# Kernel tuning notes

Hardware: AMD Instinct MI355X
Metric: run time of the kernel (lower is better)

Reference implementation:

```python
import jax, jax.numpy as jnp
import numpy as np

N_NODES = 100000
N_EDGES = 1600000
D_IN = 128
D_HID = 128
D_OUT = 32


def setup_inputs() -> dict:
    key = jax.random.key(0)
    ks = jax.random.split(key, 10)
    x = jax.random.normal(ks[0], (N_NODES, D_IN), dtype=jnp.float32)
    edge_index = jax.random.randint(ks[1], (2, N_EDGES), 0, N_NODES, dtype=jnp.int64)
    s = 0.05
    return {
        "x": x,
        "edge_index": edge_index,
        "Wl0": jax.random.normal(ks[2], (D_IN, D_HID), jnp.float32) * s,
        "bl0": jnp.zeros((D_HID,), jnp.float32),
        "Wr0": jax.random.normal(ks[3], (D_IN, D_HID), jnp.float32) * s,
        "Wl1": jax.random.normal(ks[4], (D_HID, D_HID), jnp.float32) * s,
        "bl1": jnp.zeros((D_HID,), jnp.float32),
        "Wr1": jax.random.normal(ks[5], (D_HID, D_HID), jnp.float32) * s,
        "Wl2": jax.random.normal(ks[6], (D_HID, D_OUT), jnp.float32) * s,
        "bl2": jnp.zeros((D_OUT,), jnp.float32),
        "Wr2": jax.random.normal(ks[7], (D_HID, D_OUT), jnp.float32) * s,
    }


def _sage_conv(x, src, dst, Wl, bl, Wr):
    # PyG SAGEConv (aggr='mean', root_weight=True):
    # out[i] = lin_l(mean_{j in N(i)} x_j) + lin_r(x_i)
    n = x.shape[0]
    msgs = x[src]                                        # [E, F] gather
    agg = jax.ops.segment_sum(msgs, dst, num_segments=n) # [N, F] scatter-add
    deg = jax.ops.segment_sum(jnp.ones((src.shape[0],), x.dtype), dst, num_segments=n)
    mean = agg / jnp.maximum(deg, 1.0)[:, None]
    return mean @ Wl + bl + x @ Wr


def reference(x, edge_index, Wl0, bl0, Wr0, Wl1, bl1, Wr1, Wl2, bl2, Wr2):
    src, dst = edge_index[0], edge_index[1]
    h = jax.nn.relu(_sage_conv(x, src, dst, Wl0, bl0, Wr0))
    h = jax.nn.relu(_sage_conv(h, src, dst, Wl1, bl1, Wr1))
    h = _sage_conv(h, src, dst, Wl2, bl2, Wr2)
    return jax.nn.log_softmax(h, axis=1)
```

## Files before the change

kernel.cpp:

```cpp
#include <hip/hip_runtime.h>
#include <hip/hip_bf16.h>
#include <math.h>

#define NN 100000
#define NE 1600000

#define NCB 391
#define EB  4096
#define SCT 512
#define HBK 64
#define NSB 391
#define WPB 144

typedef __attribute__((ext_vector_type(8))) short short8;
typedef __attribute__((ext_vector_type(4))) float f32x4;

__device__ __forceinline__ unsigned short f2bf(float f) {
  union { float f; unsigned int i; } v; v.f = f;
  unsigned int i = v.i;
  unsigned int r = (i + 0x7FFFu + ((i >> 16) & 1u)) >> 16;
  return (unsigned short)r;
}
__device__ __forceinline__ float bflo(unsigned int u) {
  union { unsigned int i; float f; } v; v.i = u << 16; return v.f;
}
__device__ __forceinline__ float bfhi(unsigned int u) {
  union { unsigned int i; float f; } v; v.i = u & 0xFFFF0000u; return v.f;
}
__device__ __forceinline__ float bf1(unsigned short u) {
  union { unsigned int i; float f; } v; v.i = ((unsigned int)u) << 16; return v.f;
}

__global__ __launch_bounds__(512) void k_prep(
    const int* __restrict__ dst, int* __restrict__ bcnt,
    const float* __restrict__ Wl0, const float* __restrict__ Wr0,
    const float* __restrict__ Wl1, const float* __restrict__ Wr1,
    const float* __restrict__ Wl2, const float* __restrict__ Wr2,
    unsigned short* __restrict__ B0, unsigned short* __restrict__ B1,
    unsigned short* __restrict__ B2) {
  if (blockIdx.x < HBK) {
    __shared__ int h[NCB];
    for (int i = threadIdx.x; i < NCB; i += 512) h[i] = 0;
    __syncthreads();
    int stride = HBK * 512;
    for (int e = blockIdx.x * 512 + threadIdx.x; e < NE; e += stride) {
      int d = dst[e];
      d = d < 0 ? 0 : (d >= NN ? NN - 1 : d);
      atomicAdd(&h[d >> 8], 1);
    }
    __syncthreads();
    for (int i = threadIdx.x; i < NCB; i += 512) {
      int v = h[i];
      if (v) atomicAdd(&bcnt[i], v);
    }
  } else {
    int idx = (blockIdx.x - HBK) * 512 + threadIdx.x;
    if (idx < 32768) {
      int n = idx >> 7, k = idx & 127;
      float v = (n < 128) ? Wl0[k * 128 + n] : Wr0[k * 128 + (n - 128)];
      B0[idx] = f2bf(v);
    } else if (idx < 65536) {
      int j = idx - 32768;
      int n = j >> 7, k = j & 127;
      float v = (n < 128) ? Wl1[k * 128 + n] : Wr1[k * 128 + (n - 128)];
      B1[j] = f2bf(v);
    } else if (idx < 73728) {
      int j = idx - 65536;
      int n = j >> 7, k = j & 127;
      float v = (n < 32) ? Wl2[k * 32 + n] : Wr2[k * 32 + (n - 32)];
      B2[j] = f2bf(v);
    }
  }
}

__global__ __launch_bounds__(512) void k_cscan(const int* __restrict__ bcnt,
                                               int* __restrict__ cboff,
                                               int* __restrict__ csroff) {
  __shared__ int sd[512];
  int t = threadIdx.x;
  int v = (t < NCB) ? bcnt[t] : 0;
  sd[t] = v;
  __syncthreads();
  for (int st = 1; st < 512; st <<= 1) {
    int x = (t >= st) ? sd[t - st] : 0;
    __syncthreads();
    sd[t] += x;
    __syncthreads();
  }
  if (t < NCB) cboff[t] = sd[t] - v;
  if (t == NCB - 1) { cboff[NCB] = sd[t]; csroff[NN] = sd[t]; }
}

__device__ __forceinline__ void cscatter_body(
    char* smem, int bid,
    const int* __restrict__ src, const int* __restrict__ dst,
    const int* __restrict__ cboff, int* __restrict__ ccur,
    unsigned int* __restrict__ ebuf) {
  int* lh = (int*)smem;
  unsigned int* sRank = (unsigned int*)(smem + 1600);
  unsigned int* sPay  = (unsigned int*)(smem + 1600 + EB * 4);
  int t = threadIdx.x;
  int base = bid * EB;
  for (int i = t; i < NCB; i += SCT) lh[i] = 0;
  __syncthreads();
  #pragma unroll
  for (int i = 0; i < EB / SCT; i++) {
    int idx = i * SCT + t;
    int e = base + idx;
    unsigned int rk = 0xFFFFFFFFu, pv = 0;
    if (e < NE) {
      int d = dst[e];
      d = d < 0 ? 0 : (d >= NN ? NN - 1 : d);
      int s = src[e];
      s = s < 0 ? 0 : (s >= NN ? NN - 1 : s);
      int cb = d >> 8;
      int r = atomicAdd(&lh[cb], 1);
      rk = (((unsigned int)cb) << 13) | (unsigned int)r;
      pv = (((unsigned int)(d & 255)) << 17) | (unsigned int)s;
    }
    sRank[idx] = rk;
    sPay[idx]  = pv;
  }
  __syncthreads();
  for (int i = t; i < NCB; i += SCT) {
    int c = lh[i];
    int g = c ? atomicAdd(&ccur[i], c) : 0;
    lh[i] = cboff[i] + g;
  }
  __syncthreads();
  #pragma unroll
  for (int i = 0; i < EB / SCT; i++) {
    int idx = i * SCT + t;
    unsigned int rk = sRank[idx];
    if (rk != 0xFFFFFFFFu) {
      int cb = rk >> 13;
      int r  = rk & 0x1FFF;
      ebuf[lh[cb] + r] = sPay[idx];
    }
  }
}

__device__ __forceinline__ void mgemm0_body(
    char* smem, int bid, const float* __restrict__ A,
    const unsigned short* __restrict__ Bp, const float* __restrict__ bias,
    unsigned short* __restrict__ yl, unsigned short* __restrict__ yr) {
  unsigned short* sA = (unsigned short*)smem;
  int tid = threadIdx.x;
  int nb  = bid * 128;

  #pragma unroll
  for (int i = 0; i < 8; i++) {
    int j = i * 512 + tid;
    int m = j >> 5;
    int k4 = (j & 31) * 4;
    int gn = nb + m;
    float4 v = make_float4(0.f, 0.f, 0.f, 0.f);
    if (gn < NN) v = *(const float4*)&A[gn * 128 + k4];
    unsigned int p0 = (unsigned int)f2bf(v.x) | ((unsigned int)f2bf(v.y) << 16);
    unsigned int p1 = (unsigned int)f2bf(v.z) | ((unsigned int)f2bf(v.w) << 16);
    *(uint2*)&sA[m * 136 + k4] = make_uint2(p0, p1);
  }
  __syncthreads();

  int wave = tid >> 6, lane = tid & 63;
  int l15 = lane & 15, lq = lane >> 4;
  int wm = wave & 1, wn = wave >> 1;
  int mbase = wm * 64;
  int nbase = wn * 64;

  f32x4 acc[4][4];
  #pragma unroll
  for (int mi = 0; mi < 4; mi++)
    #pragma unroll
    for (int ni = 0; ni < 4; ni++) acc[mi][ni] = (f32x4){0.f, 0.f, 0.f, 0.f};

  #pragma unroll
  for (int kc = 0; kc < 4; kc++) {
    int k0 = kc * 32 + lq * 8;
    short8 af[4], bfr[4];
    #pragma unroll
    for (int ni = 0; ni < 4; ni++)
      bfr[ni] = *(const short8*)&Bp[(nbase + ni * 16 + l15) * 128 + k0];
    #pragma unroll
    for (int mi = 0; mi < 4; mi++)
      af[mi] = *(const short8*)&sA[(mbase + mi * 16 + l15) * 136 + k0];
    #pragma unroll
    for (int mi = 0; mi < 4; mi++)
      #pragma unroll
      for (int ni = 0; ni < 4; ni++)
        acc[mi][ni] = __builtin_amdgcn_mfma_f32_16x16x32_bf16(
            af[mi], bfr[ni], acc[mi][ni], 0, 0, 0);
  }

  #pragma unroll
  for (int mi = 0; mi < 4; mi++) {
    #pragma unroll
    for (int ni = 0; ni < 4; ni++) {
      int n = nbase + ni * 16 + l15;
      #pragma unroll
      for (int r = 0; r < 4; r++) {
        int gn = nb + mbase + mi * 16 + lq * 4 + r;
        if (gn < NN) {
          float v = acc[mi][ni][r];
          if (n < 128) {
            yl[(size_t)gn * 128 + n] = f2bf(v);
          } else {
            int n2 = n - 128;
            yr[(size_t)gn * 128 + n2] = f2bf(v + bias[n2]);
          }
        }
      }
    }
  }
}

__global__ __launch_bounds__(512) void k_scatgemm(
    const int* __restrict__ src, const int* __restrict__ dst,
    const int* __restrict__ cboff, int* __restrict__ ccur,
    unsigned int* __restrict__ ebuf,
    const float* __restrict__ x, const unsigned short* __restrict__ B0,
    const float* __restrict__ bias,
    unsigned short* __restrict__ yl, unsigned short* __restrict__ yr) {
  __shared__ char smem[128 * 136 * 2];
  if (blockIdx.x < NSB) {
    cscatter_body(smem, blockIdx.x, src, dst, cboff, ccur, ebuf);
  } else {
    mgemm0_body(smem, blockIdx.x - NSB, x, B0, bias, yl, yr);
  }
}

__global__ __launch_bounds__(512) void k_crefine(
    const unsigned int* __restrict__ ebuf, const int* __restrict__ cboff,
    int* __restrict__ csroff, float* __restrict__ invd,
    int* __restrict__ csrsrc) {
  __shared__ int lh[256], pos[256], cur[256];
  int b = blockIdx.x, t = threadIdx.x;
  if (t < 256) { lh[t] = 0; cur[t] = 0; }
  __syncthreads();
  int beg = cboff[b], end = cboff[b + 1];
  for (int i = beg + t; i < end; i += 512) atomicAdd(&lh[ebuf[i] >> 17], 1);
  __syncthreads();
  int v = (t < 256) ? lh[t] : 0;
  if (t < 256) pos[t] = v;
  __syncthreads();
  for (int st = 1; st < 256; st <<= 1) {
    int x = (t >= st && t < 256) ? pos[t - st] : 0;
    __syncthreads();
    if (t < 256) pos[t] += x;
    __syncthreads();
  }
  if (t < 256) {
    int nid = b * 256 + t;
    int mybase = cboff[b] + pos[t] - v;
    if (nid < NN) {
      csroff[nid] = mybase;
      invd[nid] = 1.0f / (float)(v < 1 ? 1 : v);
    }
    pos[t] = mybase;
  }
  __syncthreads();
  for (int i = beg + t; i < end; i += 512) {
    unsigned int u = ebuf[i];
    int local = u >> 17;
    int r = atomicAdd(&cur[local], 1);
    csrsrc[pos[local] + r] = (int)(u & 0x1FFFFu);
  }
}

template <int NC>
__global__ __launch_bounds__(512) void k_mgemm(
    const unsigned short* __restrict__ A, const unsigned short* __restrict__ Bp,
    const float* __restrict__ bias,
    unsigned short* __restrict__ yl, unsigned short* __restrict__ yr) {
  __shared__ unsigned short sA[128 * 136];
  int tid = threadIdx.x;
  int nb  = blockIdx.x * 128;

  #pragma unroll
  for (int i = 0; i < 4; i++) {
    int j = i * 512 + tid;
    int m = j >> 4;
    int k8 = (j & 15) * 8;
    int gn = nb + m;
    uint4 v = make_uint4(0, 0, 0, 0);
    if (gn < NN) v = *(const uint4*)&A[gn * 128 + k8];
    *(uint4*)&sA[m * 136 + k8] = v;
  }
  __syncthreads();

  int wave = tid >> 6, lane = tid & 63;
  int l15 = lane & 15, lq = lane >> 4;
  constexpr int MT = (NC == 256) ? 4 : 2;
  constexpr int NT = (NC == 256) ? 4 : 2;
  int wm, wn;
  if (NC == 256) { wm = wave & 1; wn = wave >> 1; }
  else           { wm = wave >> 1; wn = wave & 1; }
  int mbase = wm * (MT * 16);
  int nbase = wn * (NT * 16);

  f32x4 acc[MT][NT];
  #pragma unroll
  for (int mi = 0; mi < MT; mi++)
    #pragma unroll
    for (int ni = 0; ni < NT; ni++) acc[mi][ni] = (f32x4){0.f, 0.f, 0.f, 0.f};

  #pragma unroll
  for (int kc = 0; kc < 4; kc++) {
    int k0 = kc * 32 + lq * 8;
    short8 af[MT], bfr[NT];
    #pragma unroll
    for (int ni = 0; ni < NT; ni++)
      bfr[ni] = *(const short8*)&Bp[(nbase + ni * 16 + l15) * 128 + k0];
    #pragma unroll
    for (int mi = 0; mi < MT; mi++)
      af[mi] = *(const short8*)&sA[(mbase + mi * 16 + l15) * 136 + k0];
    #pragma unroll
    for (int mi = 0; mi < MT; mi++)
      #pragma unroll
      for (int ni = 0; ni < NT; ni++)
        acc[mi][ni] = __builtin_amdgcn_mfma_f32_16x16x32_bf16(
            af[mi], bfr[ni], acc[mi][ni], 0, 0, 0);
  }

  constexpr int HC = NC / 2;
  #pragma unroll
  for (int mi = 0; mi < MT; mi++) {
    #pragma unroll
    for (int ni = 0; ni < NT; ni++) {
      int n = nbase + ni * 16 + l15;
      #pragma unroll
      for (int r = 0; r < 4; r++) {
        int gn = nb + mbase + mi * 16 + lq * 4 + r;
        if (gn < NN) {
          float v = acc[mi][ni][r];
          if (n < HC) {
            yl[(size_t)gn * HC + n] = f2bf(v);
          } else {
            int n2 = n - HC;
            yr[(size_t)gn * HC + n2] = f2bf(v + bias[n2]);
          }
        }
      }
    }
  }
}

__global__ __launch_bounds__(256) void k_agg128(
    const unsigned short* __restrict__ yl, const unsigned short* __restrict__ yr,
    const int* __restrict__ off, const int* __restrict__ csr,
    const float* __restrict__ invd, unsigned short* __restrict__ out, int relu) {
  int wid  = (blockIdx.x * 256 + threadIdx.x) >> 6;
  int lane = threadIdx.x & 63;
  if (wid >= NN) return;
  int beg = off[wid], end = off[wid + 1];
  const unsigned int* ylp = (const unsigned int*)yl;
  float ax0 = 0.f, ay0 = 0.f, ax1 = 0.f, ay1 = 0.f;
  float ax2 = 0.f, ay2 = 0.f, ax3 = 0.f, ay3 = 0.f;
  int e = beg;
  for (; e + 7 < end; e += 8) {
    int s0 = csr[e],     s1 = csr[e + 1], s2 = csr[e + 2], s3 = csr[e + 3];
    int s4 = csr[e + 4], s5 = csr[e + 5], s6 = csr[e + 6], s7 = csr[e + 7];
    unsigned int u0 = ylp[s0 * 64 + lane];
    unsigned int u1 = ylp[s1 * 64 + lane];
    unsigned int u2 = ylp[s2 * 64 + lane];
    unsigned int u3 = ylp[s3 * 64 + lane];
    unsigned int u4 = ylp[s4 * 64 + lane];
    unsigned int u5 = ylp[s5 * 64 + lane];
    unsigned int u6 = ylp[s6 * 64 + lane];
    unsigned int u7 = ylp[s7 * 64 + lane];
    ax0 += bflo(u0); ay0 += bfhi(u0);
    ax1 += bflo(u1); ay1 += bfhi(u1);
    ax2 += bflo(u2); ay2 += bfhi(u2);
    ax3 += bflo(u3); ay3 += bfhi(u3);
    ax0 += bflo(u4); ay0 += bfhi(u4);
    ax1 += bflo(u5); ay1 += bfhi(u5);
    ax2 += bflo(u6); ay2 += bfhi(u6);
    ax3 += bflo(u7); ay3 += bfhi(u7);
  }
  for (; e < end; e++) {
    int s = csr[e];
    unsigned int u = ylp[s * 64 + lane];
    ax0 += bflo(u); ay0 += bfhi(u);
  }
  float sc = invd[wid];
  unsigned int rv = ((const unsigned int*)yr)[wid * 64 + lane];
  float vx = ((ax0 + ax1) + (ax2 + ax3)) * sc + bflo(rv);
  float vy = ((ay0 + ay1) + (ay2 + ay3)) * sc + bfhi(rv);
  if (relu) { vx = fmaxf(vx, 0.f); vy = fmaxf(vy, 0.f); }
  ((unsigned int*)out)[wid * 64 + lane] =
      (unsigned int)f2bf(vx) | ((unsigned int)f2bf(vy) << 16);
}

__global__ __launch_bounds__(256) void k_agg32_lsm(
    const unsigned short* __restrict__ yl, const unsigned short* __restrict__ yr,
    const int* __restrict__ off, const int* __restrict__ csr,
    const float* __restrict__ invd, float* __restrict__ out) {
  int row  = (blockIdx.x * 256 + threadIdx.x) >> 5;
  int lane = threadIdx.x & 31;
  if (row >= NN) return;
  int beg = off[row], end = off[row + 1];
  float a0 = 0.f, a1 = 0.f, a2 = 0.f, a3 = 0.f;
  int e = beg;
  for (; e + 3 < end; e += 4) {
    int s0 = csr[e], s1 = csr[e + 1], s2 = csr[e + 2], s3 = csr[e + 3];
    a0 += bf1(yl[s0 * 32 + lane]);
    a1 += bf1(yl[s1 * 32 + lane]);
    a2 += bf1(yl[s2 * 32 + lane]);
    a3 += bf1(yl[s3 * 32 + lane]);
  }
  for (; e < end; e++) a0 += bf1(yl[csr[e] * 32 + lane]);
  float v = ((a0 + a1) + (a2 + a3)) * invd[row] + bf1(yr[row * 32 + lane]);
  float m = v;
  #pragma unroll
  for (int o = 16; o; o >>= 1) m = fmaxf(m, __shfl_xor(m, o, 32));
  float ex = expf(v - m);
  float s = ex;
  #pragma unroll
  for (int o = 16; o; o >>= 1) s += __shfl_xor(s, o, 32);
  out[row * 32 + lane] = v - m - logf(s);
}


extern "C" void kernel_launch(void* const* d_in, const int* in_sizes, int n_in,
                              void* d_out, int out_size, void* d_ws, size_t ws_size,
                              hipStream_t stream) {
  (void)in_sizes; (void)n_in; (void)out_size; (void)ws_size;
  const float* x   = (const float*)d_in[0];
  const int*   ei  = (const int*)d_in[1];
  const float* Wl0 = (const float*)d_in[2];
  const float* bl0 = (const float*)d_in[3];
  const float* Wr0 = (const float*)d_in[4];
  const float* Wl1 = (const float*)d_in[5];
  const float* bl1 = (const float*)d_in[6];
  const float* Wr1 = (const float*)d_in[7];
  const float* Wl2 = (const float*)d_in[8];
  const float* bl2 = (const float*)d_in[9];
  const float* Wr2 = (const float*)d_in[10];
  const int* srcI = ei;
  const int* dstI = ei + NE;

  char* w = (char*)d_ws;
  int*   bcnt   = (int*)(w + 0);
  int*   ccur   = (int*)(w + (4 << 10));
  int*   cboff  = (int*)(w + (32 << 10));
  unsigned short* B0 = (unsigned short*)(w + (64 << 10));
  unsigned short* B1 = (unsigned short*)(w + (160 << 10));
  unsigned short* B2 = (unsigned short*)(w + (256 << 10));
  int*   csroff = (int*)(w + (512 << 10));
  float* invd   = (float*)(w + (1024 << 10));
  unsigned int* ebuf = (unsigned int*)(w + (size_t)(2) * 1024 * 1024);
  int*   csrsrc = (int*)(w + (size_t)(9) * 1024 * 1024);
  unsigned short* ylb = (unsigned short*)(w + (size_t)(16) * 1024 * 1024);
  unsigned short* yrb = (unsigned short*)(w + (size_t)(48) * 1024 * 1024);
  unsigned short* hb  = (unsigned short*)(w + (size_t)(80) * 1024 * 1024);

  dim3 gg((NN + 127) / 128);

  hipMemsetAsync(w, 0, 8 << 10, stream);
  k_prep<<<HBK + WPB, 512, 0, stream>>>(dstI, bcnt, Wl0, Wr0, Wl1, Wr1, Wl2, Wr2,
                                        B0, B1, B2);
  k_cscan<<<1, 512, 0, stream>>>(bcnt, cboff, csroff);
  k_scatgemm<<<NSB + 782, 512, 0, stream>>>(srcI, dstI, cboff, ccur, ebuf,
                                            x, B0, bl0, ylb, yrb);
  k_crefine<<<NCB, 512, 0, stream>>>(ebuf, cboff, csroff, invd, csrsrc);
  k_agg128<<<(NN * 64) / 256, 256, 0, stream>>>(ylb, yrb, csroff, csrsrc, invd, hb, 1);
  k_mgemm<256><<<gg, 512, 0, stream>>>(hb, B1, bl1, ylb, yrb);
  k_agg128<<<(NN * 64) / 256, 256, 0, stream>>>(ylb, yrb, csroff, csrsrc, invd, hb, 1);
  k_mgemm<64><<<gg, 512, 0, stream>>>(hb, B2, bl2, ylb, yrb);
  k_agg32_lsm<<<(NN * 32) / 256, 256, 0, stream>>>(ylb, yrb, csroff, csrsrc, invd,
                                                   (float*)d_out);
}
```

Measured before the change: 452.6 us.

## Split layer-0 GEMM across scatter and refine kernels; widen agg128 edge loads

The layer-0 GEMM tiles are split so half run alongside the edge scatter and the other half run alongside the CSR refine stage in a new combined kernel. This lets the GEMM work fill idle compute during the refine pass. The 128-wide aggregation also changes so each wavefront processes two edges at once, with each half-wave loading 8 bytes per lane and the halves combined by a cross-lane shuffle. This gives fewer, wider gather loads at the cost of an extra reduction and idle half-waves on the final store.

```diff
diff --git a/kernel.cpp b/kernel.cpp
--- a/kernel.cpp
+++ b/kernel.cpp
@@ -11,6 +11,7 @@
 #define HBK 64
 #define NSB 391
 #define WPB 144
+#define GT0 391
 
 typedef __attribute__((ext_vector_type(8))) short short8;
 typedef __attribute__((ext_vector_type(4))) float f32x4;
@@ -140,6 +141,47 @@
   }
 }
 
+__device__ __forceinline__ void crefine_body(
+    char* smem, int b,
+    const unsigned int* __restrict__ ebuf, const int* __restrict__ cboff,
+    int* __restrict__ csroff, float* __restrict__ invd,
+    int* __restrict__ csrsrc) {
+  int* lh  = (int*)smem;
+  int* pos = lh + 256;
+  int* cur = pos + 256;
+  int t = threadIdx.x;
+  if (t < 256) { lh[t] = 0; cur[t] = 0; }
+  __syncthreads();
+  int beg = cboff[b], end = cboff[b + 1];
+  for (int i = beg + t; i < end; i += 512) atomicAdd(&lh[ebuf[i] >> 17], 1);
+  __syncthreads();
+  int v = (t < 256) ? lh[t] : 0;
+  if (t < 256) pos[t] = v;
+  __syncthreads();
+  for (int st = 1; st < 256; st <<= 1) {
+    int x = (t >= st && t < 256) ? pos[t - st] : 0;
+    __syncthreads();
+    if (t < 256) pos[t] += x;
+    __syncthreads();
+  }
+  if (t < 256) {
+    int nid = b * 256 + t;
+    int mybase = cboff[b] + pos[t] - v;
+    if (nid < NN) {
+      csroff[nid] = mybase;
+      invd[nid] = 1.0f / (float)(v < 1 ? 1 : v);
+    }
+    pos[t] = mybase;
+  }
+  __syncthreads();
+  for (int i = beg + t; i < end; i += 512) {
+    unsigned int u = ebuf[i];
+    int local = u >> 17;
+    int r = atomicAdd(&cur[local], 1);
+    csrsrc[pos[local] + r] = (int)(u & 0x1FFFFu);
+  }
+}
+
 __device__ __forceinline__ void mgemm0_body(
     char* smem, int bid, const float* __restrict__ A,
     const unsigned short* __restrict__ Bp, const float* __restrict__ bias,
@@ -229,41 +271,17 @@
   }
 }
 
-__global__ __launch_bounds__(512) void k_crefine(
+__global__ __launch_bounds__(512) void k_refgemm(
     const unsigned int* __restrict__ ebuf, const int* __restrict__ cboff,
-    int* __restrict__ csroff, float* __restrict__ invd,
-    int* __restrict__ csrsrc) {
-  __shared__ int lh[256], pos[256], cur[256];
-  int b = blockIdx.x, t = threadIdx.x;
-  if (t < 256) { lh[t] = 0; cur[t] = 0; }
-  __syncthreads();
-  int beg = cboff[b], end = cboff[b + 1];
-  for (int i = beg + t; i < end; i += 512) atomicAdd(&lh[ebuf[i] >> 17], 1);
-  __syncthreads();
-  int v = (t < 256) ? lh[t] : 0;
-  if (t < 256) pos[t] = v;
-  __syncthreads();
-  for (int st = 1; st < 256; st <<= 1) {
-    int x = (t >= st && t < 256) ? pos[t - st] : 0;
-    __syncthreads();
-    if (t < 256) pos[t] += x;
-    __syncthreads();
-  }
-  if (t < 256) {
-    int nid = b * 256 + t;
-    int mybase = cboff[b] + pos[t] - v;
-    if (nid < NN) {
-      csroff[nid] = mybase;
-      invd[nid] = 1.0f / (float)(v < 1 ? 1 : v);
-    }
-    pos[t] = mybase;
-  }
-  __syncthreads();
-  for (int i = beg + t; i < end; i += 512) {
-    unsigned int u = ebuf[i];
-    int local = u >> 17;
-    int r = atomicAdd(&cur[local], 1);
-    csrsrc[pos[local] + r] = (int)(u & 0x1FFFFu);
+    int* __restrict__ csroff, float* __restrict__ invd, int* __restrict__ csrsrc,
+    const float* __restrict__ x, const unsigned short* __restrict__ B0,
+    const float* __restrict__ bias,
+    unsigned short* __restrict__ yl, unsigned short* __restrict__ yr) {
+  __shared__ char smem[128 * 136 * 2];
+  if (blockIdx.x < NCB) {
+    crefine_body(smem, blockIdx.x, ebuf, cboff, csroff, invd, csrsrc);
+  } else {
+    mgemm0_body(smem, blockIdx.x - NCB + GT0, x, B0, bias, yl, yr);
   }
 }
 
@@ -352,43 +370,60 @@
   int wid  = (blockIdx.x * 256 + threadIdx.x) >> 6;
   int lane = threadIdx.x & 63;
   if (wid >= NN) return;
+  int half = lane >> 5;
+  int cp   = lane & 31;
   int beg = off[wid], end = off[wid + 1];
-  const unsigned int* ylp = (const unsigned int*)yl;
-  float ax0 = 0.f, ay0 = 0.f, ax1 = 0.f, ay1 = 0.f;
-  float ax2 = 0.f, ay2 = 0.f, ax3 = 0.f, ay3 = 0.f;
+  const uint2* ylp = (const uint2*)yl;
+  float a0 = 0.f, a1 = 0.f, a2 = 0.f, a3 = 0.f;
+  float b0 = 0.f, b1 = 0.f, b2 = 0.f, b3 = 0.f;
   int e = beg;
-  for (; e + 7 < end; e += 8) {
-    int s0 = csr[e],     s1 = csr[e + 1], s2 = csr[e + 2], s3 = csr[e + 3];
-    int s4 = csr[e + 4], s5 = csr[e + 5], s6 = csr[e + 6], s7 = csr[e + 7];
-    unsigned int u0 = ylp[s0 * 64 + lane];
-    unsigned int u1 = ylp[s1 * 64 + lane];
-    unsigned int u2 = ylp[s2 * 64 + lane];
-    unsigned int u3 = ylp[s3 * 64 + lane];
-    unsigned int u4 = ylp[s4 * 64 + lane];
-    unsigned int u5 = ylp[s5 * 64 + lane];
-    unsigned int u6 = ylp[s6 * 64 + lane];
-    unsigned int u7 = ylp[s7 * 64 + lane];
-    ax0 += bflo(u0); ay0 += bfhi(u0);
-    ax1 += bflo(u1); ay1 += bfhi(u1);
-    ax2 += bflo(u2); ay2 += bfhi(u2);
-    ax3 += bflo(u3); ay3 += bfhi(u3);
-    ax0 += bflo(u4); ay0 += bfhi(u4);
-    ax1 += bflo(u5); ay1 += bfhi(u5);
-    ax2 += bflo(u6); ay2 += bfhi(u6);
-    ax3 += bflo(u7); ay3 += bfhi(u7);
-  }
-  for (; e < end; e++) {
+  for (; e + 15 < end; e += 16) {
+    int s[8];
+    #pragma unroll
+    for (int i = 0; i < 8; i++) s[i] = csr[e + 2 * i + half];
+    uint2 u[8];
+    #pragma unroll
+    for (int i = 0; i < 8; i++) u[i] = ylp[s[i] * 32 + cp];
+    #pragma unroll
+    for (int i = 0; i < 8; i += 2) {
+      a0 += bflo(u[i].x);     a1 += bfhi(u[i].x);
+      a2 += bflo(u[i].y);     a3 += bfhi(u[i].y);
+      b0 += bflo(u[i + 1].x); b1 += bfhi(u[i + 1].x);
+      b2 += bflo(u[i + 1].y); b3 += bfhi(u[i + 1].y);
+    }
+  }
+  for (; e + 1 < end; e += 2) {
+    int s = csr[e + half];
+    uint2 u = ylp[s * 32 + cp];
+    a0 += bflo(u.x); a1 += bfhi(u.x); a2 += bflo(u.y); a3 += bfhi(u.y);
+  }
+  if (e < end) {
     int s = csr[e];
-    unsigned int u = ylp[s * 64 + lane];
-    ax0 += bflo(u); ay0 += bfhi(u);
-  }
-  float sc = invd[wid];
-  unsigned int rv = ((const unsigned int*)yr)[wid * 64 + lane];
-  float vx = ((ax0 + ax1) + (ax2 + ax3)) * sc + bflo(rv);
-  float vy = ((ay0 + ay1) + (ay2 + ay3)) * sc + bfhi(rv);
-  if (relu) { vx = fmaxf(vx, 0.f); vy = fmaxf(vy, 0.f); }
-  ((unsigned int*)out)[wid * 64 + lane] =
-      (unsigned int)f2bf(vx) | ((unsigned int)f2bf(vy) << 16);
+    uint2 u = make_uint2(0u, 0u);
+    if (half == 0) u = ylp[s * 32 + cp];
+    a0 += bflo(u.x); a1 += bfhi(u.x); a2 += bflo(u.y); a3 += bfhi(u.y);
+  }
+  a0 += b0; a1 += b1; a2 += b2; a3 += b3;
+  a0 += __shfl_xor(a0, 32);
+  a1 += __shfl_xor(a1, 32);
+  a2 += __shfl_xor(a2, 32);
+  a3 += __shfl_xor(a3, 32);
+  if (half == 0) {
+    float sc = invd[wid];
+    uint2 rv = ((const uint2*)yr)[wid * 32 + cp];
+    float v0 = a0 * sc + bflo(rv.x);
+    float v1 = a1 * sc + bfhi(rv.x);
+    float v2 = a2 * sc + bflo(rv.y);
+    float v3 = a3 * sc + bfhi(rv.y);
+    if (relu) {
+      v0 = fmaxf(v0, 0.f); v1 = fmaxf(v1, 0.f);
+      v2 = fmaxf(v2, 0.f); v3 = fmaxf(v3, 0.f);
+    }
+    uint2 o;
+    o.x = (unsigned int)f2bf(v0) | ((unsigned int)f2bf(v1) << 16);
+    o.y = (unsigned int)f2bf(v2) | ((unsigned int)f2bf(v3) << 16);
+    ((uint2*)out)[wid * 32 + cp] = o;
+  }
 }
 
 __global__ __launch_bounds__(256) void k_agg32_lsm(
@@ -460,9 +495,10 @@
   k_prep<<<HBK + WPB, 512, 0, stream>>>(dstI, bcnt, Wl0, Wr0, Wl1, Wr1, Wl2, Wr2,
                                         B0, B1, B2);
   k_cscan<<<1, 512, 0, stream>>>(bcnt, cboff, csroff);
-  k_scatgemm<<<NSB + 782, 512, 0, stream>>>(srcI, dstI, cboff, ccur, ebuf,
+  k_scatgemm<<<NSB + GT0, 512, 0, stream>>>(srcI, dstI, cboff, ccur, ebuf,
                                             x, B0, bl0, ylb, yrb);
-  k_crefine<<<NCB, 512, 0, stream>>>(ebuf, cboff, csroff, invd, csrsrc);
+  k_refgemm<<<NCB + (782 - GT0), 512, 0, stream>>>(ebuf, cboff, csroff, invd,
+                                                   csrsrc, x, B0, bl0, ylb, yrb);
   k_agg128<<<(NN * 64) / 256, 256, 0, stream>>>(ylb, yrb, csroff, csrsrc, invd, hb, 1);
   k_mgemm<256><<<gg, 512, 0, stream>>>(hb, B1, bl1, ylb, yrb);
   k_agg128<<<(NN * 64) / 256, 256, 0, stream>>>(ylb, yrb, csroff, csrsrc, invd, hb, 1);
```

Result: slower. 462.6 us (+2.2%).
